# Kernel tuning notes

Measured on AMD Instinct MI355X. Metric: run time of the kernel, lower is better.

## Reference

```python
import jax, jax.numpy as jnp
import numpy as np


def _ln(z, g, b):
    m = z.mean(-1, keepdims=True)
    v = ((z - m) ** 2).mean(-1, keepdims=True)
    return (z - m) * jax.lax.rsqrt(v + 1e-5) * g + b


def _pe(T, D):
    # standard sinusoidal positional encoding (T, D)
    pos = np.arange(T)[:, None]
    i = np.arange(D // 2)[None, :]
    ang = pos / np.power(10000.0, 2.0 * i / D)
    pe = np.zeros((T, D), dtype=np.float32)
    pe[:, 0::2] = np.sin(ang)
    pe[:, 1::2] = np.cos(ang)
    return jnp.asarray(pe)


def _whconv(z, Hinc, filt, W, b):
    # Wavelet hypergraph convolution: psi diag(filt) psi^{-1} Z W + b
    # psi = heat-kernel wavelet of normalized hypergraph Laplacian, 2nd-order Taylor (K=2, s=1)
    S = Hinc.shape[0]
    Dv = Hinc.sum(1) + 1e-6          # node degrees
    De = Hinc.sum(0) + 1e-6          # hyperedge degrees
    Hn = Hinc * (Dv ** -0.5)[:, None]
    A = (Hn / De[None, :]) @ Hn.T    # Dv^-1/2 H De^-1 H^T Dv^-1/2
    I = jnp.eye(S, dtype=z.dtype)
    L = I - A
    L2 = 0.5 * (L @ L)
    psi = I - L + L2                  # exp(-L) approx
    psi_inv = I + L + L2              # exp(+L) approx
    return psi @ (filt[:, None] * (psi_inv @ z)) @ W + b


def setup_inputs():
    S, T, F, D, NS, E, K = 2048, 64, 16, 256, 4, 128, 32
    key = jax.random.key(0)
    ks = iter(jax.random.split(key, 64))
    nrm = lambda shp: jax.random.normal(next(ks), shp, jnp.float32) * 0.02
    return dict(
        x=jax.random.normal(next(ks), (S, T, F), jnp.float32),
        snapshot=(jax.random.uniform(next(ks), (NS, S, E)) < 0.05).astype(jnp.float32),
        params_snapshot=jax.random.uniform(next(ks), (NS,), jnp.float32, 0.0, 0.99),
        beta=jnp.array([0.33, 0.33, 0.33], jnp.float32),
        W_emb=nrm((F, D)), b_emb=jnp.zeros((D,), jnp.float32),
        Wq=nrm((D, D)), bq=jnp.zeros((D,), jnp.float32),
        Wk=nrm((D, D)), bk=jnp.zeros((D,), jnp.float32),
        Wv=nrm((D, D)), bv=jnp.zeros((D,), jnp.float32),
        Wo=nrm((D, D)), bo=jnp.zeros((D,), jnp.float32),
        ln1_g=jnp.ones((D,), jnp.float32), ln1_b=jnp.zeros((D,), jnp.float32),
        W_int=nrm((D, D)), b_int=jnp.zeros((D,), jnp.float32),
        W_mix=nrm((2 * D, D)), b_mix=jnp.zeros((D,), jnp.float32),
        ln2_g=jnp.ones((D,), jnp.float32), ln2_b=jnp.zeros((D,), jnp.float32),
        Wt=nrm((D, D)), bt=jnp.zeros((D,), jnp.float32), vt=nrm((D,)),
        Wh1=nrm((D, D)), bh1=jnp.zeros((D,), jnp.float32), filt1=jnp.ones((S,), jnp.float32),
        Wh2=nrm((D, D)), bh2=jnp.zeros((D,), jnp.float32), filt2=jnp.ones((S,), jnp.float32),
        Wa=nrm((D, D)), Wb=nrm((D, D)), Wg=nrm((D, D)), bg=jnp.zeros((D,), jnp.float32),
        Wm1=nrm((D, D)), bm1=jnp.zeros((D,), jnp.float32),
        Wm2=nrm((D, 1)), bm2=jnp.zeros((1,), jnp.float32),
        num_edges=K,
    )


def reference(x, snapshot, params_snapshot, beta, W_emb, b_emb, Wq, bq, Wk, bk, Wv, bv,
              Wo, bo, ln1_g, ln1_b, W_int, b_int, W_mix, b_mix, ln2_g, ln2_b,
              Wt, bt, vt, Wh1, bh1, filt1, Wh2, bh2, filt2, Wa, Wb, Wg, bg,
              Wm1, bm1, Wm2, bm2, num_edges):
    S, T, _ = x.shape
    D = W_emb.shape[1]
    H = 8
    dh = D // H
    # feature embedding + positional encoding
    h = x @ W_emb + b_emb + _pe(T, D)
    # intra-stock (per-stock temporal) multi-head self-attention + residual + LN
    q = (h @ Wq + bq).reshape(S, T, H, dh)
    k = (h @ Wk + bk).reshape(S, T, H, dh)
    v = (h @ Wv + bv).reshape(S, T, H, dh)
    att = jax.nn.softmax(jnp.einsum('sqhd,skhd->shqk', q, k) / jnp.sqrt(jnp.float32(dh)), axis=-1)
    o = jnp.einsum('shqk,skhd->sqhd', att, v).reshape(S, T, D) @ Wo + bo
    h = _ln(h + o, ln1_g, ln1_b)
    # intensity function + mixing layer (Linear -> ReLU -> LayerNorm)
    intensity = jax.nn.softplus(h @ W_int + b_int)
    z = jax.nn.relu(jnp.concatenate([h, intensity], axis=-1) @ W_mix + b_mix)
    h = _ln(z, ln2_g, ln2_b)
    # temporal attention pooling: (S,T,D) -> (S,D)
    u = jnp.tanh(h @ Wt + bt)
    a = jax.nn.softmax(u @ vt, axis=-1)          # (S,T)
    xs = jnp.einsum('st,std->sd', a, h)           # (S,D)
    # per-snapshot two-layer wavelet hypergraph conv (dropout = eval identity)
    def per_snap(Hinc):
        r1 = jax.nn.leaky_relu(_whconv(xs, Hinc, filt1, Wh1, bh1), 0.1)
        return _whconv(r1, Hinc, filt2, Wh2, bh2)
    reps = jax.vmap(per_snap)(snapshot)           # (NS,S,D)
    hyper = jnp.einsum('n,nsd->sd', params_snapshot, reps)
    # dynamic graph learning: top-k learned similarity graph
    sim = (xs @ Wa) @ (xs @ Wb).T / jnp.sqrt(jnp.float32(D))
    kth = jax.lax.top_k(sim, num_edges)[0][:, -1]
    Adyn = jax.nn.softmax(jnp.where(sim >= kth[:, None], sim, -jnp.inf), axis=-1)
    dyn = jax.nn.relu(Adyn @ xs @ Wg + bg)
    # fusion ('sum' mode) + MLP head
    w = jax.nn.softmax(beta)
    fused = w[0] * xs + w[1] * dyn + w[2] * hyper
    return jax.nn.relu(fused @ Wm1 + bm1) @ Wm2 + bm2   # (S,1)
```

## Files before the change

kernel.cpp:

```cpp
#include <hip/hip_runtime.h>
#include <math.h>

#define S_ 2048
#define T_ 64
#define F_ 16
#define D_ 256
#define NS_ 4
#define E_ 128
#define H_ 8
#define SD_ (S_*D_)
#define PS 264

#define PK_ATT 0
#define PK_WO  393216
#define PK_WI  524288
#define PK_WT  655360
#define PK_WM  786432
#define PKBASE 11674112
#define PK2BASE 5242880
#define PKH1 0
#define PKH2 131072
#define PKA  262144
#define PKB  393216
#define PKG  524288
#define PKM1 655360

typedef __attribute__((ext_vector_type(8))) short bf16x8;
typedef __attribute__((ext_vector_type(4))) float f32x4;

__device__ __forceinline__ float warp_sum64(float v){
  #pragma unroll
  for (int o=32;o>=1;o>>=1) v += __shfl_xor(v,o);
  return v;
}
__device__ __forceinline__ float warp_max64(float v){
  #pragma unroll
  for (int o=32;o>=1;o>>=1) v = fmaxf(v,__shfl_xor(v,o));
  return v;
}
__device__ __forceinline__ float softplus_f(float v){
  return fmaxf(v,0.f) + log1pf(__expf(-fabsf(v)));
}
__device__ __forceinline__ float tanh_f(float v){
  float t = __expf(-2.f*fabsf(v));
  float r = (1.f-t)/(1.f+t);
  return copysignf(r, v);
}
__device__ __forceinline__ void splitf(float f, short& h, short& l){
  unsigned u = __float_as_uint(f);
  unsigned hb = (u + 0x7FFFu + ((u>>16)&1u)) >> 16;
  float fl = f - __uint_as_float(hb<<16);
  unsigned v = __float_as_uint(fl);
  unsigned lb = (v + 0x7FFFu + ((v>>16)&1u)) >> 16;
  h = (short)hb; l = (short)lb;
}
__device__ __forceinline__ f32x4 mfma3(bf16x8 ah, bf16x8 al, bf16x8 bh, bf16x8 bl, f32x4 c){
  c = __builtin_amdgcn_mfma_f32_16x16x32_bf16(al, bh, c, 0,0,0);
  c = __builtin_amdgcn_mfma_f32_16x16x32_bf16(ah, bl, c, 0,0,0);
  c = __builtin_amdgcn_mfma_f32_16x16x32_bf16(ah, bh, c, 0,0,0);
  return c;
}
__device__ __forceinline__ void afrag_f32(const float* base, int stride, int rbase, int ks, int lane, bf16x8& hi, bf16x8& lo){
  const float* p = base + (rbase + (lane&15))*stride + ks + ((lane>>4)<<3);
  #pragma unroll
  for (int jj=0;jj<8;++jj){ short h,l; splitf(p[jj],h,l); hi[jj]=h; lo[jj]=l; }
}
__device__ __forceinline__ bf16x8 afrag_pk(const short* plane, int rbase, int ks, int lane){
  return *(const bf16x8*)(plane + (rbase + (lane&15))*PS + ks + ((lane>>4)<<3));
}
__device__ __forceinline__ void bfrag_pk(const unsigned* pk, int tile, int lane, bf16x8& hi, bf16x8& lo){
  const unsigned* p = pk + (((tile<<6) + lane)<<3);
  #pragma unroll
  for (int jj=0;jj<8;++jj){ unsigned u=p[jj]; hi[jj]=(short)(u & 0xffffu); lo[jj]=(short)(u>>16); }
}
__device__ __forceinline__ void store_h(short* Hh, short* Hl, int r, int c, float f){
  short h,l; splitf(f,h,l);
  Hh[r*PS+c]=h; Hl[r*PS+c]=l;
}
__device__ __forceinline__ float load_h(const short* Hh, const short* Hl, int r, int c){
  int idx=r*PS+c;
  return __uint_as_float(((unsigned)(unsigned short)Hh[idx])<<16)
       + __uint_as_float(((unsigned)(unsigned short)Hl[idx])<<16);
}

__global__ void pack_all(const float* __restrict__ Wq, const float* __restrict__ Wk,
                         const float* __restrict__ Wv, const float* __restrict__ Wo,
                         const float* __restrict__ Wint, const float* __restrict__ Wt,
                         const float* __restrict__ Wmix,
                         const float* __restrict__ Wh1, const float* __restrict__ Wh2,
                         const float* __restrict__ Wa, const float* __restrict__ Wb,
                         const float* __restrict__ Wg, const float* __restrict__ Wm1,
                         short* __restrict__ pkc, short* __restrict__ pk2){
  int y = blockIdx.y;
  int i = blockIdx.x*256 + threadIdx.x;
  if (y < 3){
    const float* W = (y==0)?Wq:((y==1)?Wk:Wv);
    int jj=i&7, n=(i>>3)&15, q=(i>>7)&3, ntg=(i>>9)&15, kt=i>>13;
    float f = W[(kt*32 + q*8 + jj)*256 + (ntg*16+n)];
    short h,l; splitf(f,h,l);
    int hp = ntg>>2, ntl = ntg&3;
    int base = ((hp*8+kt)*6 + y*2)*2048;
    int local = ntl*512 + (q*16+n)*8 + jj;
    short* dst = pkc + PK_ATT;
    dst[base+local] = h;
    dst[base+2048+local] = l;
  } else {
    const float* W; short* dst; int ib = i;
    if (y==3){W=Wo;   dst=pkc+PK_WO;}
    else if (y==4){W=Wint; dst=pkc+PK_WI;}
    else if (y==5){W=Wt;   dst=pkc+PK_WT;}
    else if (y==6){W=Wmix; dst=pkc+PK_WM;}
    else if (y==7){W=Wmix; dst=pkc+PK_WM; ib = i + 65536;}
    else if (y==8){W=Wh1;  dst=pk2+PKH1;}
    else if (y==9){W=Wh2;  dst=pk2+PKH2;}
    else if (y==10){W=Wa;  dst=pk2+PKA;}
    else if (y==11){W=Wb;  dst=pk2+PKB;}
    else if (y==12){W=Wg;  dst=pk2+PKG;}
    else          {W=Wm1;  dst=pk2+PKM1;}
    int jj=ib&7, n=(ib>>3)&15, q=(ib>>7)&3, ntg=(ib>>9)&15, kt=ib>>13;
    float f = W[(kt*32 + q*8 + jj)*256 + (ntg*16+n)];
    short h,l; splitf(f,h,l);
    int dl = kt*16384 + ntg*512 + (q*16+n)*8 + jj;
    dst[dl] = h; dst[dl+8192] = l;
  }
}

__global__ void pe_kernel(float* __restrict__ pe){
  int i = blockIdx.x*256 + threadIdx.x;
  int t = i >> 8, d = i & 255;
  int ii = d >> 1;
  float w = __expf(-(float)ii * (logf(10000.f)/128.f));
  float ang = (float)t * w;
  pe[i] = (d & 1) ? cosf(ang) : sinf(ang);
}

__launch_bounds__(512,1)
__global__ void stageA_kernel(
    const float* __restrict__ x, const float* __restrict__ pe,
    const float* __restrict__ Wemb, const float* __restrict__ bemb,
    const float* __restrict__ bq, const float* __restrict__ bk, const float* __restrict__ bv,
    const float* __restrict__ bo,
    const float* __restrict__ ln1g, const float* __restrict__ ln1b,
    const float* __restrict__ bint,
    const float* __restrict__ bmix,
    const float* __restrict__ ln2g, const float* __restrict__ ln2b,
    const float* __restrict__ bt,
    const float* __restrict__ vt,
    const short* __restrict__ pkc,
    float* __restrict__ xs)
{
  __shared__ __attribute__((aligned(16))) short hbh[64*PS];
  __shared__ __attribute__((aligned(16))) short hbl[64*PS];
  __shared__ __attribute__((aligned(16))) char smem[85504];

  short*    wst   = (short*)smem;
  unsigned* k2f2  = (unsigned*)smem;
  unsigned* v2f2  = (unsigned*)(smem + 16384);
  float*    qb2   = (float*)(smem + 32768);
  float*    scb2  = (float*)(smem + 50176);
  float*    poolb = (float*)smem;

  const int j  = threadIdx.x;
  const int s  = blockIdx.x;
  const int w  = j >> 6;
  const int lane = j & 63;
  const int m_ = lane & 15, qd = lane >> 4;
  const int rg2 = w >> 1, par = w & 1;
  const int rbase = rg2*16;
  const int rv = w*8;
  const int c0 = lane;

  {
    float* xb = (float*)smem;
    const float* xp = x + (long)s*T_*F_;
    for (int i=j; i<T_*F_; i+=512) xb[i] = xp[i];
  }
  __syncthreads();

  {
    const float* xb = (const float*)smem;
    float acc[8][4];
    #pragma unroll
    for (int r=0;r<8;++r){acc[r][0]=0;acc[r][1]=0;acc[r][2]=0;acc[r][3]=0;}
    #pragma unroll
    for (int k=0;k<F_;++k){
      float w0=Wemb[k*D_+c0], w1=Wemb[k*D_+c0+64], w2=Wemb[k*D_+c0+128], w3=Wemb[k*D_+c0+192];
      #pragma unroll
      for (int r=0;r<8;++r){
        float hv = xb[(rv+r)*F_+k];
        acc[r][0]+=hv*w0; acc[r][1]+=hv*w1; acc[r][2]+=hv*w2; acc[r][3]+=hv*w3;
      }
    }
    float b0=bemb[c0],b1=bemb[c0+64],b2=bemb[c0+128],b3=bemb[c0+192];
    __syncthreads();
    #pragma unroll
    for (int r=0;r<8;++r){
      int t = rv+r;
      store_h(hbh,hbl,t,c0,     acc[r][0]+b0+pe[t*D_+c0]);
      store_h(hbh,hbl,t,c0+64,  acc[r][1]+b1+pe[t*D_+c0+64]);
      store_h(hbh,hbl,t,c0+128, acc[r][2]+b2+pe[t*D_+c0+128]);
      store_h(hbh,hbl,t,c0+192, acc[r][3]+b3+pe[t*D_+c0+192]);
    }
  }
  __syncthreads();

  bf16x8 AH[8], AL[8];
  #pragma unroll
  for (int kt=0;kt<8;++kt){
    AH[kt] = afrag_pk(hbh, rbase, kt*32, lane);
    AL[kt] = afrag_pk(hbl, rbase, kt*32, lane);
  }

  const float rs = 0.17677669529663687f;
  f32x4 co[8];
  #pragma unroll
  for (int t=0;t<8;++t) co[t] = (f32x4){0.f,0.f,0.f,0.f};

  for (int hp=0; hp<4; ++hp){
    f32x4 qa[2],ka[2],va[2];
    #pragma unroll
    for (int t=0;t<2;++t){
      qa[t]=(f32x4){0.f,0.f,0.f,0.f};
      ka[t]=(f32x4){0.f,0.f,0.f,0.f};
      va[t]=(f32x4){0.f,0.f,0.f,0.f};
    }
    bf16x8 pre[3];
    {
      const short* b0 = pkc + PK_ATT + (hp*8)*12288;
      #pragma unroll
      for (int r=0;r<3;++r) pre[r] = *(const bf16x8*)(b0 + (j+r*512)*8);
    }
    for (int kt=0; kt<8; ++kt){
      __syncthreads();
      #pragma unroll
      for (int r=0;r<3;++r) *(bf16x8*)(wst + (j+r*512)*8) = pre[r];
      __syncthreads();
      if (kt<7){
        const short* nb = pkc + PK_ATT + (hp*8+kt+1)*12288;
        #pragma unroll
        for (int r=0;r<3;++r) pre[r] = *(const bf16x8*)(nb + (j+r*512)*8);
      }
      bf16x8 ah = AH[kt], al = AL[kt];
      #pragma unroll
      for (int t=0;t<2;++t){
        int ntl = par*2+t;
        bf16x8 bh,bl;
        bh = *(bf16x8*)(wst +         ntl*512 + lane*8);
        bl = *(bf16x8*)(wst + 2048  + ntl*512 + lane*8);
        qa[t]=mfma3(ah,al,bh,bl,qa[t]);
        bh = *(bf16x8*)(wst + 4096  + ntl*512 + lane*8);
        bl = *(bf16x8*)(wst + 6144  + ntl*512 + lane*8);
        ka[t]=mfma3(ah,al,bh,bl,ka[t]);
        bh = *(bf16x8*)(wst + 8192  + ntl*512 + lane*8);
        bl = *(bf16x8*)(wst + 10240 + ntl*512 + lane*8);
        va[t]=mfma3(ah,al,bh,bl,va[t]);
      }
    }
    __syncthreads();
    #pragma unroll
    for (int t=0;t<2;++t){
      int ntg = par*2+t;
      #pragma unroll
      for (int r=0;r<4;++r){
        int trow = rbase + qd*4 + r;
        int pcp = ntg*16 + m_;
        int head = pcp >> 5;
        int cp = pcp & 31;
        int col = hp*64 + pcp;
        qb2[trow*68 + pcp] = (qa[t][r] + bq[col]) * rs;
        short hS,lS;
        float kv2 = ka[t][r] + bk[col];
        splitf(kv2,hS,lS);
        k2f2[head*2048 + (((trow>>4)*4 + (cp>>3))*16 + (trow&15))*8 + (cp&7)]
            = (unsigned)(unsigned short)hS | ((unsigned)(unsigned short)lS<<16);
        float vv2 = va[t][r] + bv[col];
        splitf(vv2,hS,lS);
        v2f2[head*2048 + ((((trow>>5)*2 + (cp>>4))*4 + ((trow>>3)&3))*16 + (cp&15))*8 + (trow&7)]
            = (unsigned)(unsigned short)hS | ((unsigned)(unsigned short)lS<<16);
      }
    }
    __syncthreads();
    float* scb = scb2 + par*4352;
    {
      bf16x8 ah,al;
      afrag_f32(qb2, 68, rbase, par*32, lane, ah, al);
      f32x4 sc4[4];
      #pragma unroll
      for (int nt=0;nt<4;++nt){
        bf16x8 bh,bl; bfrag_pk(k2f2 + par*2048, nt, lane, bh, bl);
        sc4[nt] = mfma3(ah,al,bh,bl,(f32x4){0.f,0.f,0.f,0.f});
      }
      #pragma unroll
      for (int r=0;r<4;++r){
        float mx = fmaxf(fmaxf(sc4[0][r],sc4[1][r]),fmaxf(sc4[2][r],sc4[3][r]));
        #pragma unroll
        for (int o=8;o>=1;o>>=1) mx = fmaxf(mx, __shfl_xor(mx,o));
        float es = 0.f;
        #pragma unroll
        for (int nt=0;nt<4;++nt){ float e=__expf(sc4[nt][r]-mx); sc4[nt][r]=e; es+=e; }
        #pragma unroll
        for (int o=8;o>=1;o>>=1) es += __shfl_xor(es,o);
        float inv = 1.f/es;
        int trow = rbase + qd*4 + r;
        #pragma unroll
        for (int nt=0;nt<4;++nt) scb[trow*68 + nt*16 + m_] = sc4[nt][r]*inv;
      }
    }
    {
      f32x4 oa[2];
      oa[0]=(f32x4){0.f,0.f,0.f,0.f}; oa[1]=(f32x4){0.f,0.f,0.f,0.f};
      #pragma unroll
      for (int kt=0;kt<2;++kt){
        bf16x8 ah2,al2; afrag_f32(scb, 68, rbase, kt*32, lane, ah2, al2);
        #pragma unroll
        for (int nt=0;nt<2;++nt){
          bf16x8 bh,bl; bfrag_pk(v2f2 + par*2048, kt*2+nt, lane, bh, bl);
          oa[nt]=mfma3(ah2,al2,bh,bl,oa[nt]);
        }
      }
      #pragma unroll
      for (int nt=0;nt<2;++nt){
        #pragma unroll
        for (int r=0;r<4;++r)
          qb2[(rbase+qd*4+r)*68 + par*32 + nt*16 + m_] = oa[nt][r];
      }
    }
    __syncthreads();
    for (int ks=0; ks<2; ++ks){
      bf16x8 ah,al; afrag_f32(qb2, 68, rbase, ks*32, lane, ah, al);
      const short* wob = pkc + PK_WO + (hp*2+ks)*16384 + lane*8;
      #pragma unroll
      for (int t=0;t<8;++t){
        int ntg = 2*t+par;
        bf16x8 bh = *(const bf16x8*)(wob + ntg*512);
        bf16x8 bl = *(const bf16x8*)(wob + 8192 + ntg*512);
        co[t]=mfma3(ah,al,bh,bl,co[t]);
      }
    }
  }

  #pragma unroll
  for (int t=0;t<8;++t){
    int cc = (2*t+par)*16+m_;
    float bov = bo[cc];
    #pragma unroll
    for (int r=0;r<4;++r){
      int row = rbase+qd*4+r;
      store_h(hbh,hbl,row,cc, load_h(hbh,hbl,row,cc) + co[t][r] + bov);
    }
  }
  __syncthreads();

  {
    float g0=ln1g[c0],g1=ln1g[c0+64],g2=ln1g[c0+128],g3=ln1g[c0+192];
    float bb0=ln1b[c0],bb1=ln1b[c0+64],bb2=ln1b[c0+128],bb3=ln1b[c0+192];
    for (int rr=0;rr<8;++rr){
      int t=rv+rr;
      float v0=load_h(hbh,hbl,t,c0),    v1=load_h(hbh,hbl,t,c0+64);
      float v2=load_h(hbh,hbl,t,c0+128),v3=load_h(hbh,hbl,t,c0+192);
      float sm=warp_sum64(v0+v1+v2+v3);
      float sq=warp_sum64(v0*v0+v1*v1+v2*v2+v3*v3);
      float mean=sm*(1.f/256.f);
      float inv=rsqrtf(fmaxf(sq*(1.f/256.f)-mean*mean,0.f)+1e-5f);
      store_h(hbh,hbl,t,c0,    (v0-mean)*inv*g0+bb0);
      store_h(hbh,hbl,t,c0+64, (v1-mean)*inv*g1+bb1);
      store_h(hbh,hbl,t,c0+128,(v2-mean)*inv*g2+bb2);
      store_h(hbh,hbl,t,c0+192,(v3-mean)*inv*g3+bb3);
    }
  }
  __syncthreads();

  auto loadB=[&](bf16x8* d, const short* base, int kt){
    const short* p = base + kt*16384 + lane*8;
    d[0]=*(const bf16x8*)(p + (2*w)*512);
    d[1]=*(const bf16x8*)(p + 8192 + (2*w)*512);
    d[2]=*(const bf16x8*)(p + (2*w+1)*512);
    d[3]=*(const bf16x8*)(p + 8192 + (2*w+1)*512);
  };
  const short* BM = pkc + PK_WM;
  const short* BI = pkc + PK_WI;
  const short* BT = pkc + PK_WT;

  f32x4 az[4][2], ai[4][2];
  #pragma unroll
  for (int rt=0;rt<4;++rt){
    az[rt][0]=(f32x4){0.f,0.f,0.f,0.f}; az[rt][1]=(f32x4){0.f,0.f,0.f,0.f};
    ai[rt][0]=(f32x4){0.f,0.f,0.f,0.f}; ai[rt][1]=(f32x4){0.f,0.f,0.f,0.f};
  }
  bf16x8 cb[4], nb[4];
  loadB(cb, BM, 0);
  for (int kt=0; kt<8; ++kt){
    if (kt<7) loadB(nb, BM, kt+1); else loadB(nb, BI, 0);
    #pragma unroll
    for (int rt=0;rt<4;++rt){
      bf16x8 ah = afrag_pk(hbh, rt*16, kt*32, lane);
      bf16x8 al = afrag_pk(hbl, rt*16, kt*32, lane);
      az[rt][0]=mfma3(ah,al,cb[0],cb[1],az[rt][0]);
      az[rt][1]=mfma3(ah,al,cb[2],cb[3],az[rt][1]);
    }
    #pragma unroll
    for (int r=0;r<4;++r) cb[r]=nb[r];
  }
  for (int kt=0; kt<8; ++kt){
    if (kt<7) loadB(nb, BI, kt+1); else loadB(nb, BM, 8);
    #pragma unroll
    for (int rt=0;rt<4;++rt){
      bf16x8 ah = afrag_pk(hbh, rt*16, kt*32, lane);
      bf16x8 al = afrag_pk(hbl, rt*16, kt*32, lane);
      ai[rt][0]=mfma3(ah,al,cb[0],cb[1],ai[rt][0]);
      ai[rt][1]=mfma3(ah,al,cb[2],cb[3],ai[rt][1]);
    }
    #pragma unroll
    for (int r=0;r<4;++r) cb[r]=nb[r];
  }
  __syncthreads();
  #pragma unroll
  for (int rt=0;rt<4;++rt){
    #pragma unroll
    for (int t=0;t<2;++t){
      int col=(2*w+t)*16+m_;
      float bb=bint[col];
      #pragma unroll
      for (int r=0;r<4;++r)
        store_h(hbh,hbl, rt*16+qd*4+r, col, softplus_f(ai[rt][t][r]+bb));
    }
  }
  __syncthreads();
  for (int kt=0; kt<8; ++kt){
    if (kt<7) loadB(nb, BM, kt+9); else loadB(nb, BT, 0);
    #pragma unroll
    for (int rt=0;rt<4;++rt){
      bf16x8 ah = afrag_pk(hbh, rt*16, kt*32, lane);
      bf16x8 al = afrag_pk(hbl, rt*16, kt*32, lane);
      az[rt][0]=mfma3(ah,al,cb[0],cb[1],az[rt][0]);
      az[rt][1]=mfma3(ah,al,cb[2],cb[3],az[rt][1]);
    }
    #pragma unroll
    for (int r=0;r<4;++r) cb[r]=nb[r];
  }
  __syncthreads();
  #pragma unroll
  for (int rt=0;rt<4;++rt){
    #pragma unroll
    for (int t=0;t<2;++t){
      int col=(2*w+t)*16+m_;
      float bb=bmix[col];
      #pragma unroll
      for (int r=0;r<4;++r)
        store_h(hbh,hbl, rt*16+qd*4+r, col, fmaxf(az[rt][t][r]+bb,0.f));
    }
  }
  __syncthreads();
  {
    float g0=ln2g[c0],g1=ln2g[c0+64],g2=ln2g[c0+128],g3=ln2g[c0+192];
    float bb0=ln2b[c0],bb1=ln2b[c0+64],bb2=ln2b[c0+128],bb3=ln2b[c0+192];
    for (int rr=0;rr<8;++rr){
      int t=rv+rr;
      float v0=load_h(hbh,hbl,t,c0),    v1=load_h(hbh,hbl,t,c0+64);
      float v2=load_h(hbh,hbl,t,c0+128),v3=load_h(hbh,hbl,t,c0+192);
      float sm=warp_sum64(v0+v1+v2+v3);
      float sq=warp_sum64(v0*v0+v1*v1+v2*v2+v3*v3);
      float mean=sm*(1.f/256.f);
      float inv=rsqrtf(fmaxf(sq*(1.f/256.f)-mean*mean,0.f)+1e-5f);
      store_h(hbh,hbl,t,c0,    (v0-mean)*inv*g0+bb0);
      store_h(hbh,hbl,t,c0+64, (v1-mean)*inv*g1+bb1);
      store_h(hbh,hbl,t,c0+128,(v2-mean)*inv*g2+bb2);
      store_h(hbh,hbl,t,c0+192,(v3-mean)*inv*g3+bb3);
    }
  }
  __syncthreads();
  {
    f32x4 at4[4][2];
    #pragma unroll
    for (int rt=0;rt<4;++rt){
      at4[rt][0]=(f32x4){0.f,0.f,0.f,0.f}; at4[rt][1]=(f32x4){0.f,0.f,0.f,0.f};
    }
    for (int kt=0; kt<8; ++kt){
      if (kt<7) loadB(nb, BT, kt+1);
      #pragma unroll
      for (int rt=0;rt<4;++rt){
        bf16x8 ah = afrag_pk(hbh, rt*16, kt*32, lane);
        bf16x8 al = afrag_pk(hbl, rt*16, kt*32, lane);
        at4[rt][0]=mfma3(ah,al,cb[0],cb[1],at4[rt][0]);
        at4[rt][1]=mfma3(ah,al,cb[2],cb[3],at4[rt][1]);
      }
      #pragma unroll
      for (int r=0;r<4;++r) cb[r]=nb[r];
    }
    #pragma unroll
    for (int rt=0;rt<4;++rt){
      #pragma unroll
      for (int r=0;r<4;++r){
        int row = rt*16+qd*4+r;
        float p = 0.f;
        #pragma unroll
        for (int t=0;t<2;++t){
          int col=(2*w+t)*16+m_;
          p += tanh_f(at4[rt][t][r]+bt[col])*vt[col];
        }
        p += __shfl_xor(p,1); p += __shfl_xor(p,2);
        p += __shfl_xor(p,4); p += __shfl_xor(p,8);
        if (m_==0) poolb[w*64+row] = p;
      }
    }
  }
  __syncthreads();
  if (j < 64){
    float v = 0.f;
    #pragma unroll
    for (int ww=0;ww<8;++ww) v += poolb[ww*64+j];
    float m = warp_max64(v);
    float e = __expf(v-m);
    float ssum = warp_sum64(e);
    poolb[512+j] = e/ssum;
  }
  __syncthreads();
  if (j < 256){
    float acc=0.f;
    #pragma unroll 8
    for (int t=0;t<T_;++t) acc += poolb[512+t]*load_h(hbh,hbl,t,j);
    xs[(long)s*D_+j] = acc;
  }
}

__global__ void hg_deg(const float* __restrict__ Hinc, float* __restrict__ Dv, float* __restrict__ De){
  const int n = blockIdx.y, s0 = blockIdx.x*64;
  const float* Hp = Hinc + (long)n*S_*E_;
  const int j = threadIdx.x;
  {
    int r = j>>2, q = j&3;
    const float* rp = Hp + (long)(s0+r)*E_ + q*32;
    float sm=0;
    #pragma unroll
    for (int e=0;e<32;++e) sm += rp[e];
    sm += __shfl_xor(sm,1); sm += __shfl_xor(sm,2);
    if (q==0) Dv[n*S_+s0+r]=sm+1e-6f;
  }
  if (j < E_){
    float cs=0;
    for (int ss=0;ss<64;++ss) cs += Hp[(long)(s0+ss)*E_+j];
    atomicAdd(&De[n*E_+j], cs);
  }
}

__global__ void build_ecsr(const float* __restrict__ snap, const float* __restrict__ Dv,
                           int* __restrict__ ei, float* __restrict__ ev, int* __restrict__ ecnt){
  __shared__ int cnts[257];
  const int e = blockIdx.x, n = blockIdx.y, t = threadIdx.x;
  const float* col = snap + (long)n*S_*E_ + e;
  int loc[8]; int c=0;
  #pragma unroll
  for (int r=0;r<8;++r){
    int s = t*8+r;
    if (col[(long)s*E_] != 0.f) loc[c++]=s;
  }
  cnts[t+1]=c;
  __syncthreads();
  if (t==0){ cnts[0]=0; for (int i=1;i<=256;++i) cnts[i]+=cnts[i-1]; }
  __syncthreads();
  int base = cnts[t];
  long eb = ((long)n*E_+e)*256;
  for (int k=0;k<c;++k){
    int pos = base+k;
    if (pos<256){ ei[eb+pos]=loc[k]; ev[eb+pos]=rsqrtf(Dv[n*S_+loc[k]]); }
  }
  if (t==255) ecnt[n*E_+e] = min(cnts[256],256);
}
__global__ void build_scsr(const float* __restrict__ snap, const float* __restrict__ Dv,
                           const float* __restrict__ De,
                           int* __restrict__ si, float* __restrict__ sv, int* __restrict__ scnt){
  const int s = blockIdx.x*256+threadIdx.x, n = blockIdx.y;
  const float* row = snap + ((long)n*S_+s)*E_;
  float vs = rsqrtf(Dv[n*S_+s]);
  long sb = ((long)n*S_+s)*32;
  int c=0;
  for (int e=0;e<E_;++e){
    if (row[e]!=0.f && c<32){
      si[sb+c]=e;
      sv[sb+c]=vs/(De[n*E_+e]+1e-6f);
      ++c;
    }
  }
  scnt[n*S_+s]=c;
}

__launch_bounds__(256,4)
__global__ void hg_p1(const int* __restrict__ ei, const float* __restrict__ ev,
                      const int* __restrict__ ecnt,
                      const float* __restrict__ M, long mz, float* __restrict__ P){
  __shared__ int sidx[256];
  __shared__ float sval[256];
  const int e = blockIdx.x, n = blockIdx.y, d = threadIdx.x;
  long eb = ((long)n*E_+e)*256;
  const int c = ecnt[n*E_+e];
  if (d < c){ sidx[d]=ei[eb+d]; sval[d]=ev[eb+d]; }
  __syncthreads();
  const float* Mp = M + (long)n*mz;
  float a0=0.f,a1=0.f,a2=0.f,a3=0.f;
  int i=0;
  for (; i+4<=c; i+=4){
    float m0 = Mp[(long)sidx[i+0]*D_+d];
    float m1 = Mp[(long)sidx[i+1]*D_+d];
    float m2 = Mp[(long)sidx[i+2]*D_+d];
    float m3 = Mp[(long)sidx[i+3]*D_+d];
    a0 += sval[i+0]*m0; a1 += sval[i+1]*m1;
    a2 += sval[i+2]*m2; a3 += sval[i+3]*m3;
  }
  for (; i<c; ++i) a0 += sval[i]*Mp[(long)sidx[i]*D_+d];
  P[((long)n*E_+e)*D_+d] = (a0+a1)+(a2+a3);
}
__launch_bounds__(256,4)
__global__ void hg_p2(const int* __restrict__ si, const float* __restrict__ sv,
                      const int* __restrict__ scnt, const float* __restrict__ P,
                      const float* __restrict__ X1, long x1z, float c1,
                      const float* __restrict__ X2, long x2z, float c2,
                      float c3, const float* __restrict__ filt, int usefilt,
                      float* __restrict__ out){
  __shared__ int sidx[8][32];
  __shared__ float sval[8][32];
  __shared__ int scc[8];
  const int s0 = blockIdx.x*8, n = blockIdx.y, d = threadIdx.x;
  {
    int k = d>>5, i = d&31;
    long sb = ((long)n*S_+s0+k)*32;
    sidx[k][i] = si[sb+i];
    sval[k][i] = sv[sb+i];
    if (i==0) scc[k] = scnt[n*S_+s0+k];
  }
  __syncthreads();
  const float* Pn = P + (long)n*E_*D_;
  #pragma unroll
  for (int k=0;k<8;++k){
    int s = s0+k;
    int c = scc[k];
    float acc=0.f;
    for (int i=0;i<c;++i) acc += sval[k][i]*Pn[(long)sidx[k][i]*D_+d];
    long li=(long)s*D_+d;
    float v=c3*acc;
    if (X1) v+=c1*X1[x1z*n+li];
    if (X2) v+=c2*X2[x2z*n+li];
    out[((long)n*S_+s)*D_+d]=(usefilt?filt[s]:1.f)*v;
  }
}

__launch_bounds__(256,4)
__global__ void gemm_pk(const float* __restrict__ A, const short* __restrict__ Bpk,
                        float* __restrict__ C, const float* __restrict__ bias, int act)
{
  const int j = threadIdx.x;
  const int w = j>>6, lane = j&63;
  const int m_ = lane&15, qd = lane>>4;
  const long r0 = (long)blockIdx.x*64 + w*16;
  f32x4 acc[16];
  #pragma unroll
  for (int nt=0;nt<16;++nt) acc[nt]=(f32x4){0.f,0.f,0.f,0.f};
  #pragma unroll
  for (int kt=0; kt<8; ++kt){
    bf16x8 ah, al;
    {
      const float* p = A + (r0 + m_)*D_ + kt*32 + (qd<<3);
      #pragma unroll
      for (int jj=0;jj<8;++jj){ short h,l; splitf(p[jj],h,l); ah[jj]=h; al[jj]=l; }
    }
    const short* bp = Bpk + kt*16384 + lane*8;
    #pragma unroll
    for (int nt=0;nt<16;++nt){
      bf16x8 bh = *(const bf16x8*)(bp + nt*512);
      bf16x8 bl = *(const bf16x8*)(bp + 8192 + nt*512);
      acc[nt]=mfma3(ah,al,bh,bl,acc[nt]);
    }
  }
  #pragma unroll
  for (int nt=0;nt<16;++nt){
    int col = nt*16+m_;
    float bb = bias ? bias[col] : 0.f;
    #pragma unroll
    for (int r=0;r<4;++r){
      float v = acc[nt][r]+bb;
      if (act==1) v=fmaxf(v,0.f);
      else if (act==2) v=(v>0.f)?v:0.1f*v;
      C[(r0+qd*4+r)*D_ + col] = v;
    }
  }
}

__launch_bounds__(256,4)
__global__ void gemm_nt_pk(const float* __restrict__ A, const float* __restrict__ B,
                           float* __restrict__ C, float scale)
{
  const int j = threadIdx.x;
  const int w = j>>6, lane = j&63;
  const int m_ = lane&15, qd = lane>>4;
  const long r0 = (long)blockIdx.x*64 + w*16;
  const long c0 = (long)blockIdx.y*64;
  f32x4 acc[4];
  #pragma unroll
  for (int nt=0;nt<4;++nt) acc[nt]=(f32x4){0.f,0.f,0.f,0.f};
  #pragma unroll
  for (int kt=0; kt<8; ++kt){
    bf16x8 ah, al;
    {
      const float* p = A + (r0 + m_)*D_ + kt*32 + (qd<<3);
      #pragma unroll
      for (int jj=0;jj<8;++jj){ short h,l; splitf(p[jj],h,l); ah[jj]=h; al[jj]=l; }
    }
    #pragma unroll
    for (int nt=0;nt<4;++nt){
      bf16x8 bh, bl;
      const float* p = B + (c0 + nt*16 + m_)*D_ + kt*32 + (qd<<3);
      #pragma unroll
      for (int jj=0;jj<8;++jj){ short h,l; splitf(p[jj],h,l); bh[jj]=h; bl[jj]=l; }
      acc[nt]=mfma3(ah,al,bh,bl,acc[nt]);
    }
  }
  #pragma unroll
  for (int nt=0;nt<4;++nt){
    #pragma unroll
    for (int r=0;r<4;++r)
      C[(r0+qd*4+r)*S_ + c0 + nt*16 + m_] = acc[nt][r]*scale;
  }
}

__launch_bounds__(256,4)
__global__ void topk_gather(const float* __restrict__ sim, const float* __restrict__ xs,
                            const int* __restrict__ Kp, float* __restrict__ dynpre)
{
  __shared__ float wred[4]; __shared__ int ired[4];
  __shared__ float selw[256]; __shared__ int seli[256];
  __shared__ int cnt; __shared__ float sh_kth, sh_max, sh_den; __shared__ int sh_bi;
  const int s = blockIdx.x, j = threadIdx.x;
  const float* rp = sim + (long)s*S_;
  float vo[8], v[8];
  *(float4*)&vo[0] = *(const float4*)&rp[j*8];
  *(float4*)&vo[4] = *(const float4*)&rp[j*8+4];
  #pragma unroll
  for (int r=0;r<8;++r) v[r]=vo[r];
  if (j==0) cnt=0;
  const int K = Kp[0];
  for (int it=0; it<K; ++it){
    float m=-3.0e38f; int mi=0;
    #pragma unroll
    for (int r=0;r<8;++r){ if (v[r]>m){m=v[r]; mi=r;} }
    mi += j*8;
    #pragma unroll
    for (int o=32;o>=1;o>>=1){
      float om=__shfl_xor(m,o); int oi=__shfl_xor(mi,o);
      if (om>m){m=om;mi=oi;}
    }
    if ((j&63)==0){ wred[j>>6]=m; ired[j>>6]=mi; }
    __syncthreads();
    if (j==0){
      float bm=wred[0]; int bi=ired[0];
      #pragma unroll
      for (int w=1;w<4;++w) if (wred[w]>bm){bm=wred[w];bi=ired[w];}
      sh_kth=bm; sh_bi=bi;
      if (it==0) sh_max=bm;
    }
    __syncthreads();
    int sel = sh_bi - j*8;
    #pragma unroll
    for (int r=0;r<8;++r) if (r==sel) v[r] = -3.0e38f;
  }
  const float kth=sh_kth, rmax=sh_max;
  #pragma unroll
  for (int r=0;r<8;++r){
    if (vo[r]>=kth){
      int p=atomicAdd(&cnt,1);
      if (p<256){ seli[p]=j*8+r; selw[p]=__expf(vo[r]-rmax); }
    }
  }
  __syncthreads();
  int c = cnt; if (c>256) c=256;
  {
    float p = (j<c)? selw[j] : 0.f;
    p = warp_sum64(p);
    if ((j&63)==0) wred[j>>6]=p;
    __syncthreads();
    if (j==0) sh_den = wred[0]+wred[1]+wred[2]+wred[3];
    __syncthreads();
  }
  float acc=0.f;
  for (int l=0;l<c;++l) acc += selw[l]*xs[(long)seli[l]*D_ + j];
  dynpre[(long)s*D_+j] = acc / sh_den;
}

__global__ void hyperwsum_kernel(const float* __restrict__ reps, const float* __restrict__ ps,
                                 float* __restrict__ hyper)
{
  long idx = (long)blockIdx.x*256+threadIdx.x;
  hyper[idx] = ps[0]*reps[idx] + ps[1]*reps[(long)SD_+idx]
             + ps[2]*reps[2L*SD_+idx] + ps[3]*reps[3L*SD_+idx];
}

__global__ void fuse_kernel(const float* __restrict__ xs, const float* __restrict__ dyn,
                            const float* __restrict__ hyper, const float* __restrict__ beta,
                            float* __restrict__ fused)
{
  long idx = (long)blockIdx.x*256+threadIdx.x;
  float b0=beta[0],b1=beta[1],b2=beta[2];
  float mx=fmaxf(b0,fmaxf(b1,b2));
  float e0=__expf(b0-mx),e1=__expf(b1-mx),e2=__expf(b2-mx);
  float inv=1.f/(e0+e1+e2);
  fused[idx] = e0*inv*xs[idx] + e1*inv*dyn[idx] + e2*inv*hyper[idx];
}

__global__ void head_kernel(const float* __restrict__ hh1, const float* __restrict__ Wm2,
                            const float* __restrict__ bm2, float* __restrict__ out)
{
  int r = blockIdx.x*32 + (threadIdx.x>>3);
  int sub = threadIdx.x&7;
  const float* hp = hh1 + (long)r*D_;
  float acc=0.f;
  for (int c=sub;c<D_;c+=8) acc += hp[c]*Wm2[c];
  acc += __shfl_xor(acc,1); acc += __shfl_xor(acc,2); acc += __shfl_xor(acc,4);
  if (sub==0) out[r]=acc+bm2[0];
}

extern "C" void kernel_launch(void* const* d_in, const int* in_sizes, int n_in,
                              void* d_out, int out_size, void* d_ws, size_t ws_size,
                              hipStream_t stream)
{
  (void)in_sizes;(void)n_in;(void)out_size;(void)ws_size;
  const float* x        =(const float*)d_in[0];
  const float* snapshot =(const float*)d_in[1];
  const float* ps       =(const float*)d_in[2];
  const float* beta     =(const float*)d_in[3];
  const float* Wemb=(const float*)d_in[4];  const float* bemb=(const float*)d_in[5];
  const float* Wq  =(const float*)d_in[6];  const float* bq  =(const float*)d_in[7];
  const float* Wk  =(const float*)d_in[8];  const float* bk  =(const float*)d_in[9];
  const float* Wv  =(const float*)d_in[10]; const float* bv  =(const float*)d_in[11];
  const float* Wo  =(const float*)d_in[12]; const float* bo  =(const float*)d_in[13];
  const float* ln1g=(const float*)d_in[14]; const float* ln1b=(const float*)d_in[15];
  const float* Wint=(const float*)d_in[16]; const float* bint=(const float*)d_in[17];
  const float* Wmix=(const float*)d_in[18]; const float* bmix=(const float*)d_in[19];
  const float* ln2g=(const float*)d_in[20]; const float* ln2b=(const float*)d_in[21];
  const float* Wt  =(const float*)d_in[22]; const float* bt  =(const float*)d_in[23];
  const float* vt  =(const float*)d_in[24];
  const float* Wh1 =(const float*)d_in[25]; const float* bh1 =(const float*)d_in[26];
  const float* filt1=(const float*)d_in[27];
  const float* Wh2 =(const float*)d_in[28]; const float* bh2 =(const float*)d_in[29];
  const float* filt2=(const float*)d_in[30];
  const float* Wa  =(const float*)d_in[31]; const float* Wb  =(const float*)d_in[32];
  const float* Wg  =(const float*)d_in[33]; const float* bg  =(const float*)d_in[34];
  const float* Wm1 =(const float*)d_in[35]; const float* bm1 =(const float*)d_in[36];
  const float* Wm2 =(const float*)d_in[37]; const float* bm2 =(const float*)d_in[38];
  const int* numedges=(const int*)d_in[39];
  float* out=(float*)d_out;

  float* w = (float*)d_ws;
  float* pe    = w;
  float* repsb = w;
  float* sim   = w;
  float* P     = w + 4194304;
  float* Dv    = P + 131072;
  float* De    = Dv + 8192;
  int*   ecnt  = (int*)(De + 512);
  int*   scnt  = ecnt + 512;
  int*   ei    = scnt + 8192;
  float* ev    = (float*)(ei + 131072);
  int*   si    = (int*)(ev + 131072);
  float* sv    = (float*)(si + 262144);
  short* pk2   = (short*)(w + PK2BASE);
  float* xs    = w + 6431232;
  float* hyper = xs + SD_;
  float* bufA  = hyper + SD_;
  float* bufB  = bufA + 4*SD_;
  float* p1    = bufA;
  float* q1    = bufA + SD_;
  float* dynpre= bufA + 2*SD_;
  float* dyn   = bufA + 3*SD_;
  float* fused = bufB;
  float* hh1   = bufB + SD_;
  short* pkc   = (short*)(w + PKBASE);

  hipMemsetAsync(De, 0, (size_t)NS_*E_*sizeof(float), stream);
  pe_kernel<<<64,256,0,stream>>>(pe);
  pack_all<<<dim3(256,14),256,0,stream>>>(Wq,Wk,Wv,Wo,Wint,Wt,Wmix,
                                          Wh1,Wh2,Wa,Wb,Wg,Wm1,pkc,pk2);

  stageA_kernel<<<S_,512,0,stream>>>(x,pe,Wemb,bemb,bq,bk,bv,bo,
                                     ln1g,ln1b,bint,bmix,ln2g,ln2b,bt,vt,
                                     pkc,xs);
  hg_deg<<<dim3(32,NS_),256,0,stream>>>(snapshot,Dv,De);
  build_ecsr<<<dim3(E_,NS_),256,0,stream>>>(snapshot,Dv,ei,ev,ecnt);
  build_scsr<<<dim3(8,NS_),256,0,stream>>>(snapshot,Dv,De,si,sv,scnt);

  auto applyA=[&](const float* M, long mz,
                  const float* X1, long x1z, float c1,
                  const float* X2, long x2z, float c2, float c3,
                  const float* filt, int uf, float* outb){
    hg_p1<<<dim3(E_,NS_),256,0,stream>>>(ei,ev,ecnt,M,mz,P);
    hg_p2<<<dim3(S_/8,NS_),256,0,stream>>>(si,sv,scnt,P,X1,x1z,c1,X2,x2z,c2,c3,filt,uf,outb);
  };

  applyA(xs,0,     xs,0,1.f,    nullptr,0,0.f,  -1.f,  nullptr,0, bufA);
  applyA(bufA,SD_, xs,0,1.f,    bufA,SD_,1.5f,  -0.5f, filt1,1,   bufB);
  applyA(bufB,SD_, bufB,SD_,1.f, nullptr,0,0.f, -1.f,  nullptr,0, bufA);
  applyA(bufA,SD_, bufB,SD_,1.f, bufA,SD_,-0.5f,-0.5f, nullptr,0, bufA);
  gemm_pk<<<128,256,0,stream>>>(bufA, pk2+PKH1, bufB, bh1, 2);

  applyA(bufB,SD_, bufB,SD_,1.f, nullptr,0,0.f, -1.f,  nullptr,0, bufA);
  applyA(bufA,SD_, bufB,SD_,1.f, bufA,SD_,1.5f, -0.5f, filt2,1,   bufB);
  applyA(bufB,SD_, bufB,SD_,1.f, nullptr,0,0.f, -1.f,  nullptr,0, bufA);
  applyA(bufA,SD_, bufB,SD_,1.f, bufA,SD_,-0.5f,-0.5f, nullptr,0, bufA);
  gemm_pk<<<128,256,0,stream>>>(bufA, pk2+PKH2, repsb, bh2, 0);
  hyperwsum_kernel<<<2048,256,0,stream>>>(repsb,ps,hyper);

  gemm_pk<<<32,256,0,stream>>>(xs, pk2+PKA, p1, nullptr, 0);
  gemm_pk<<<32,256,0,stream>>>(xs, pk2+PKB, q1, nullptr, 0);
  gemm_nt_pk<<<dim3(32,32),256,0,stream>>>(p1,q1,sim,0.0625f);
  topk_gather<<<S_,256,0,stream>>>(sim,xs,numedges,dynpre);
  gemm_pk<<<32,256,0,stream>>>(dynpre, pk2+PKG, dyn, bg, 1);

  fuse_kernel<<<2048,256,0,stream>>>(xs,dyn,hyper,beta,fused);
  gemm_pk<<<32,256,0,stream>>>(fused, pk2+PKM1, hh1, bm1, 1);
  head_kernel<<<64,256,0,stream>>>(hh1,Wm2,bm2,out);
}
```

Before: 1.548 ms.

## Split gemm_pk over column blocks and pre-split p1/q1 into bf16 hi/lo

gemm_pk now launches four column-block groups via blockIdx.y, so each block computes 4 of the 16 column tiles. This raises the grid from 32/128 blocks to 128/512 for the small GEMMs. The p1/q1 projections now write bf16 hi/lo halves directly, and a new gemm_nt_pk2 loads these pre-split operands instead of re-splitting fp32 values inside the S×S similarity GEMM. The cost is that the A-row split is now repeated four times across column blocks, and the workspace needs new buffers for the packed halves.

Result: faster. 1.433 ms (-7.4%).

```diff
diff --git a/kernel.cpp b/kernel.cpp
--- a/kernel.cpp
+++ b/kernel.cpp
@@ -645,15 +645,17 @@
 
 __launch_bounds__(256,4)
 __global__ void gemm_pk(const float* __restrict__ A, const short* __restrict__ Bpk,
-                        float* __restrict__ C, const float* __restrict__ bias, int act)
+                        float* __restrict__ C, short* __restrict__ Ch, short* __restrict__ Cl,
+                        const float* __restrict__ bias, int act)
 {
   const int j = threadIdx.x;
   const int w = j>>6, lane = j&63;
   const int m_ = lane&15, qd = lane>>4;
   const long r0 = (long)blockIdx.x*64 + w*16;
-  f32x4 acc[16];
-  #pragma unroll
-  for (int nt=0;nt<16;++nt) acc[nt]=(f32x4){0.f,0.f,0.f,0.f};
+  const int nb = blockIdx.y*4;
+  f32x4 acc[4];
+  #pragma unroll
+  for (int t=0;t<4;++t) acc[t]=(f32x4){0.f,0.f,0.f,0.f};
   #pragma unroll
   for (int kt=0; kt<8; ++kt){
     bf16x8 ah, al;
@@ -664,29 +666,32 @@
     }
     const short* bp = Bpk + kt*16384 + lane*8;
     #pragma unroll
-    for (int nt=0;nt<16;++nt){
-      bf16x8 bh = *(const bf16x8*)(bp + nt*512);
-      bf16x8 bl = *(const bf16x8*)(bp + 8192 + nt*512);
-      acc[nt]=mfma3(ah,al,bh,bl,acc[nt]);
-    }
-  }
-  #pragma unroll
-  for (int nt=0;nt<16;++nt){
-    int col = nt*16+m_;
+    for (int t=0;t<4;++t){
+      bf16x8 bh = *(const bf16x8*)(bp + (nb+t)*512);
+      bf16x8 bl = *(const bf16x8*)(bp + 8192 + (nb+t)*512);
+      acc[t]=mfma3(ah,al,bh,bl,acc[t]);
+    }
+  }
+  #pragma unroll
+  for (int t=0;t<4;++t){
+    int col = (nb+t)*16+m_;
     float bb = bias ? bias[col] : 0.f;
     #pragma unroll
     for (int r=0;r<4;++r){
-      float v = acc[nt][r]+bb;
+      float v = acc[t][r]+bb;
       if (act==1) v=fmaxf(v,0.f);
       else if (act==2) v=(v>0.f)?v:0.1f*v;
-      C[(r0+qd*4+r)*D_ + col] = v;
+      long idx = (r0+qd*4+r)*D_ + col;
+      if (C) C[idx]=v;
+      else { short h,l; splitf(v,h,l); Ch[idx]=h; Cl[idx]=l; }
     }
   }
 }
 
 __launch_bounds__(256,4)
-__global__ void gemm_nt_pk(const float* __restrict__ A, const float* __restrict__ B,
-                           float* __restrict__ C, float scale)
+__global__ void gemm_nt_pk2(const short* __restrict__ Ah, const short* __restrict__ Al,
+                            const short* __restrict__ Bh, const short* __restrict__ Bl,
+                            float* __restrict__ C, float scale)
 {
   const int j = threadIdx.x;
   const int w = j>>6, lane = j&63;
@@ -698,18 +703,13 @@
   for (int nt=0;nt<4;++nt) acc[nt]=(f32x4){0.f,0.f,0.f,0.f};
   #pragma unroll
   for (int kt=0; kt<8; ++kt){
-    bf16x8 ah, al;
-    {
-      const float* p = A + (r0 + m_)*D_ + kt*32 + (qd<<3);
-      #pragma unroll
-      for (int jj=0;jj<8;++jj){ short h,l; splitf(p[jj],h,l); ah[jj]=h; al[jj]=l; }
-    }
+    int ko = kt*32 + (qd<<3);
+    bf16x8 ah = *(const bf16x8*)(Ah + (r0+m_)*D_ + ko);
+    bf16x8 al = *(const bf16x8*)(Al + (r0+m_)*D_ + ko);
     #pragma unroll
     for (int nt=0;nt<4;++nt){
-      bf16x8 bh, bl;
-      const float* p = B + (c0 + nt*16 + m_)*D_ + kt*32 + (qd<<3);
-      #pragma unroll
-      for (int jj=0;jj<8;++jj){ short h,l; splitf(p[jj],h,l); bh[jj]=h; bl[jj]=l; }
+      bf16x8 bh = *(const bf16x8*)(Bh + (c0+nt*16+m_)*D_ + ko);
+      bf16x8 bl = *(const bf16x8*)(Bl + (c0+nt*16+m_)*D_ + ko);
       acc[nt]=mfma3(ah,al,bh,bl,acc[nt]);
     }
   }
@@ -860,13 +860,15 @@
   float* ev    = (float*)(ei + 131072);
   int*   si    = (int*)(ev + 131072);
   float* sv    = (float*)(si + 262144);
+  short* p1h   = (short*)(w + 4342784);
+  short* p1l   = p1h + 524288;
   short* pk2   = (short*)(w + PK2BASE);
+  short* q1h   = (short*)(w + 5636096);
+  short* q1l   = q1h + 524288;
   float* xs    = w + 6431232;
   float* hyper = xs + SD_;
   float* bufA  = hyper + SD_;
   float* bufB  = bufA + 4*SD_;
-  float* p1    = bufA;
-  float* q1    = bufA + SD_;
   float* dynpre= bufA + 2*SD_;
   float* dyn   = bufA + 3*SD_;
   float* fused = bufB;
@@ -897,22 +899,22 @@
   applyA(bufA,SD_, xs,0,1.f,    bufA,SD_,1.5f,  -0.5f, filt1,1,   bufB);
   applyA(bufB,SD_, bufB,SD_,1.f, nullptr,0,0.f, -1.f,  nullptr,0, bufA);
   applyA(bufA,SD_, bufB,SD_,1.f, bufA,SD_,-0.5f,-0.5f, nullptr,0, bufA);
-  gemm_pk<<<128,256,0,stream>>>(bufA, pk2+PKH1, bufB, bh1, 2);
+  gemm_pk<<<dim3(128,4),256,0,stream>>>(bufA, pk2+PKH1, bufB, nullptr,nullptr, bh1, 2);
 
   applyA(bufB,SD_, bufB,SD_,1.f, nullptr,0,0.f, -1.f,  nullptr,0, bufA);
   applyA(bufA,SD_, bufB,SD_,1.f, bufA,SD_,1.5f, -0.5f, filt2,1,   bufB);
   applyA(bufB,SD_, bufB,SD_,1.f, nullptr,0,0.f, -1.f,  nullptr,0, bufA);
   applyA(bufA,SD_, bufB,SD_,1.f, bufA,SD_,-0.5f,-0.5f, nullptr,0, bufA);
-  gemm_pk<<<128,256,0,stream>>>(bufA, pk2+PKH2, repsb, bh2, 0);
+  gemm_pk<<<dim3(128,4),256,0,stream>>>(bufA, pk2+PKH2, repsb, nullptr,nullptr, bh2, 0);
   hyperwsum_kernel<<<2048,256,0,stream>>>(repsb,ps,hyper);
 
-  gemm_pk<<<32,256,0,stream>>>(xs, pk2+PKA, p1, nullptr, 0);
-  gemm_pk<<<32,256,0,stream>>>(xs, pk2+PKB, q1, nullptr, 0);
-  gemm_nt_pk<<<dim3(32,32),256,0,stream>>>(p1,q1,sim,0.0625f);
+  gemm_pk<<<dim3(32,4),256,0,stream>>>(xs, pk2+PKA, nullptr, p1h, p1l, nullptr, 0);
+  gemm_pk<<<dim3(32,4),256,0,stream>>>(xs, pk2+PKB, nullptr, q1h, q1l, nullptr, 0);
+  gemm_nt_pk2<<<dim3(32,32),256,0,stream>>>(p1h,p1l,q1h,q1l,sim,0.0625f);
   topk_gather<<<S_,256,0,stream>>>(sim,xs,numedges,dynpre);
-  gemm_pk<<<32,256,0,stream>>>(dynpre, pk2+PKG, dyn, bg, 1);
+  gemm_pk<<<dim3(32,4),256,0,stream>>>(dynpre, pk2+PKG, dyn, nullptr,nullptr, bg, 1);
 
   fuse_kernel<<<2048,256,0,stream>>>(xs,dyn,hyper,beta,fused);
-  gemm_pk<<<32,256,0,stream>>>(fused, pk2+PKM1, hh1, bm1, 1);
+  gemm_pk<<<dim3(32,4),256,0,stream>>>(fused, pk2+PKM1, hh1, nullptr,nullptr, bm1, 1);
   head_kernel<<<64,256,0,stream>>>(hh1,Wm2,bm2,out);
 }
```
